# Kernel optimization log

Hardware: AMD Instinct MI355X
Metric: run time of the kernel (lower is better)

## Reference

```python
import jax, jax.numpy as jnp
import numpy as np

EPS = 1e-6
NHEADS = 16


def setup_inputs() -> dict:
    key = jax.random.key(0)
    ks = jax.random.split(key, 6)
    b, n, dim, h = 2, 2048, 2048, NHEADS
    d = dim // h
    x = jax.random.normal(ks[0], (b, n, dim), dtype=jnp.float32)
    qkv_w = jax.random.normal(ks[1], (3 * dim, dim), dtype=jnp.float32) * (dim ** -0.5)
    qkv_b = jax.random.normal(ks[2], (3 * dim,), dtype=jnp.float32) * 0.01
    q_norm_w = jnp.ones((d,), dtype=jnp.float32)
    k_norm_w = jnp.ones((d,), dtype=jnp.float32)
    # Flux-style rotation matrices: (1, 1, n, d/2, 2, 2)
    pos = jnp.arange(n, dtype=jnp.float32)[:, None]
    inv_freq = 1.0 / (10000.0 ** (jnp.arange(0, d, 2, dtype=jnp.float32) / d))  # [d/2]
    ang = pos * inv_freq[None, :]  # [n, d/2]
    cos, sin = jnp.cos(ang), jnp.sin(ang)
    rot = jnp.stack([jnp.stack([cos, -sin], axis=-1),
                     jnp.stack([sin, cos], axis=-1)], axis=-1)  # [n, d/2, 2, 2]
    rot = rot[None, None]  # [1,1,n,d/2,2,2]
    return {"x": x, "qkv_w": qkv_w, "qkv_b": qkv_b,
            "q_norm_w": q_norm_w, "k_norm_w": k_norm_w, "rot": rot}


def _rmsnorm(t, w):
    t32 = t.astype(jnp.float32)
    inv = jax.lax.rsqrt(jnp.mean(t32 * t32, axis=-1, keepdims=True) + EPS)
    return ((t32 * inv) * w).astype(t.dtype)


def _apply_rope(t, rot):
    # t: [b,h,n,d]; rot: [1,1,n,d/2,2,2]
    b, h, n, d = t.shape
    tx = t.astype(jnp.float32).reshape(b, h, n, d // 2, 1, 2)
    out = rot[..., 0] * tx[..., 0] + rot[..., 1] * tx[..., 1]  # [b,h,n,d/2,2]
    return out.reshape(b, h, n, d).astype(t.dtype)


def reference(x, qkv_w, qkv_b, q_norm_w, k_norm_w, rot):
    b, n, dim = x.shape
    d = q_norm_w.shape[0]
    h = dim // d
    qkv = x @ qkv_w.T + qkv_b  # [b, n, 3*dim]
    # layout per Rearrange 'b n (h d j) -> b h n d j'
    qkv = qkv.reshape(b, n, h, d, 3).transpose(0, 2, 1, 3, 4)  # [b,h,n,d,3]
    q, k, v = qkv[..., 0], qkv[..., 1], qkv[..., 2]
    q = _apply_rope(_rmsnorm(q, q_norm_w), rot)
    k = _apply_rope(_rmsnorm(k, k_norm_w), rot)
    scores = jnp.einsum('bhqd,bhkd->bhqk', q, k) * (d ** -0.5)
    attn = jax.nn.softmax(scores, axis=-1)
    out = jnp.einsum('bhqk,bhkd->bhqd', attn, v)
    return out.transpose(0, 2, 1, 3).reshape(b, n, dim)  # b n (h d)
```

## Files before the change

kernel.cpp:

```cpp
#include <hip/hip_runtime.h>
#include <cstdint>
#include <cstddef>


#define LOG2E 1.4426950408889634f
#define ATT_SCALE 0.08838834764831845f
#define QSCALE (ATT_SCALE * LOG2E)

typedef __attribute__((ext_vector_type(8))) __bf16 bf16x8;
typedef __attribute__((ext_vector_type(4))) __bf16 bf16x4;
typedef __attribute__((ext_vector_type(4))) float f32x4;

__device__ __forceinline__ float b2f(unsigned u) {
  u <<= 16;
  return __builtin_bit_cast(float, u);
}
__device__ __forceinline__ unsigned short f2b(float f) {
  unsigned x = __builtin_bit_cast(unsigned, f);
  return (unsigned short)((x + 0x7fffu + ((x >> 16) & 1u)) >> 16);
}
__device__ __forceinline__ void gl16(const void* g, void* l) {
  __builtin_amdgcn_global_load_lds((__attribute__((address_space(1))) void*)(g),
                                   (__attribute__((address_space(3))) void*)(l), 16, 0, 0);
}

__global__ void k_cvt(const float4* __restrict__ in, ushort4* __restrict__ out, int n4) {
  int i = blockIdx.x * blockDim.x + threadIdx.x;
  int st = gridDim.x * blockDim.x;
  for (; i < n4; i += st) {
    float4 v = in[i];
    ushort4 o;
    o.x = f2b(v.x); o.y = f2b(v.y); o.z = f2b(v.z); o.w = f2b(v.w);
    out[i] = o;
  }
}

__global__ __launch_bounds__(512, 2) void k_gemm(const unsigned short* __restrict__ A,
                                                 const unsigned short* __restrict__ W,
                                                 const float* __restrict__ bias,
                                                 unsigned short* __restrict__ C) {
  __shared__ __align__(16) unsigned short lds[65536];
  const int tid = threadIdx.x;
  const int w = tid >> 6, l = tid & 63;
  const int lo = l & 15, hi = l >> 4;
  const int WM = w >> 2, WN = w & 3;
  const int wg = blockIdx.x;
  const int swz = (wg & 7) * 64 + (wg >> 3);
  const int mbase = (swz >> 4) * 128, nbase = (swz & 15) * 384;

  const int srow = w * 16 + (l >> 2);
  const int scol = ((l & 3) * 8) ^ (((srow >> 1) & 3) << 3);

  auto stage = [&](int t, int slot) {
    unsigned short* Sa = lds + slot * 16384;
    unsigned short* Sb = Sa + 4096;
    const int kt = t * 32;
    gl16(A + (size_t)(mbase + srow) * 2048 + kt + scol,
         Sa + (w * 16) * 32);
#pragma unroll
    for (int rd = 0; rd < 3; ++rd)
      gl16(W + (size_t)(nbase + rd * 128 + srow) * 2048 + kt + scol,
           Sb + (rd * 128 + w * 16) * 32);
  };

  f32x4 acc[4][6] = {};
  stage(0, 0); stage(1, 1); stage(2, 2);

  const int ea = (hi * 8) ^ (((lo >> 1) & 3) << 3);
  for (int t = 0; t < 64; ++t) {
    if (t < 62)       asm volatile("s_waitcnt vmcnt(8) lgkmcnt(0)" ::: "memory");
    else if (t == 62) asm volatile("s_waitcnt vmcnt(4) lgkmcnt(0)" ::: "memory");
    else              asm volatile("s_waitcnt vmcnt(0) lgkmcnt(0)" ::: "memory");
    __builtin_amdgcn_sched_barrier(0);
    __builtin_amdgcn_s_barrier();
    __builtin_amdgcn_sched_barrier(0);
    if (t + 3 < 64) stage(t + 3, (t + 3) & 3);

    const unsigned short* Sa = lds + (t & 3) * 16384;
    const unsigned short* Sb = Sa + 4096;
    bf16x8 af[4], bf[6];
#pragma unroll
    for (int i = 0; i < 4; ++i)
      af[i] = *(const bf16x8*)&Sa[(WM * 64 + i * 16 + lo) * 32 + ea];
#pragma unroll
    for (int j = 0; j < 6; ++j)
      bf[j] = *(const bf16x8*)&Sb[(WN * 96 + j * 16 + lo) * 32 + ea];

    __builtin_amdgcn_s_setprio(1);
#pragma unroll
    for (int i = 0; i < 4; ++i)
#pragma unroll
      for (int j = 0; j < 6; ++j)
        acc[i][j] = __builtin_amdgcn_mfma_f32_16x16x32_bf16(af[i], bf[j], acc[i][j], 0, 0, 0);
    __builtin_amdgcn_s_setprio(0);
  }

  const int rowb = mbase + WM * 64;
  const int colb = nbase + WN * 96;
#pragma unroll
  for (int j = 0; j < 6; ++j) {
    float bj = bias[colb + j * 16 + lo];
#pragma unroll
    for (int i = 0; i < 4; ++i)
#pragma unroll
      for (int r = 0; r < 4; ++r) {
        int row = rowb + i * 16 + hi * 4 + r;
        C[(size_t)row * 6144 + colb + j * 16 + lo] = f2b(acc[i][j][r] + bj);
      }
  }
}

__global__ __launch_bounds__(256) void k_normrope(const unsigned short* __restrict__ qkv,
                                                  const float* __restrict__ qw,
                                                  const float* __restrict__ kw,
                                                  const float* __restrict__ rot,
                                                  unsigned short* __restrict__ Q,
                                                  unsigned short* __restrict__ K,
                                                  unsigned short* __restrict__ V) {
  const int l = threadIdx.x & 63;
  const int idx = blockIdx.x * 4 + (threadIdx.x >> 6);
  const int h = idx & 15;
  const int n = (idx >> 4) & 2047;
  const int b = idx >> 15;
  const unsigned* p = (const unsigned*)(qkv + (size_t)(b * 2048 + n) * 6144 + h * 384 + l * 6);
  unsigned u0 = p[0], u1 = p[1], u2 = p[2];
  float q0 = b2f(u0 & 0xffff), k0 = b2f(u0 >> 16);
  float v0 = b2f(u1 & 0xffff), q1 = b2f(u1 >> 16);
  float k1 = b2f(u2 & 0xffff), v1 = b2f(u2 >> 16);
  (void)v0; (void)v1;
  float sq = q0 * q0 + q1 * q1, sk = k0 * k0 + k1 * k1;
#pragma unroll
  for (int m = 1; m < 64; m <<= 1) {
    sq += __shfl_xor(sq, m, 64);
    sk += __shfl_xor(sk, m, 64);
  }
  float qi = rsqrtf(sq * (1.0f / 128.0f) + 1e-6f) * QSCALE;
  float ki = rsqrtf(sk * (1.0f / 128.0f) + 1e-6f);
  float2 qwv = *(const float2*)&qw[2 * l];
  float2 kwv = *(const float2*)&kw[2 * l];
  float4 r = *(const float4*)&rot[n * 256 + l * 4];
  float qn0 = q0 * qi * qwv.x, qn1 = q1 * qi * qwv.y;
  float kn0 = k0 * ki * kwv.x, kn1 = k1 * ki * kwv.y;
  unsigned qo = (unsigned)f2b(r.x * qn0 + r.y * qn1) | ((unsigned)f2b(r.z * qn0 + r.w * qn1) << 16);
  unsigned ko = (unsigned)f2b(r.x * kn0 + r.y * kn1) | ((unsigned)f2b(r.z * kn0 + r.w * kn1) << 16);
  unsigned vo = (u1 & 0xffffu) | (u2 & 0xffff0000u);
  size_t ob = ((size_t)(b * 16 + h) * 2048 + n) * 128 + 2 * l;
  *(unsigned*)(Q + ob) = qo;
  *(unsigned*)(K + ob) = ko;
  *(unsigned*)(V + ob) = vo;
}

__global__ __launch_bounds__(256) void k_transpose(const unsigned short* __restrict__ V,
                                                   unsigned short* __restrict__ Vt) {
  __shared__ unsigned short tile[64 * 66];
  const int t = threadIdx.x;
  const int d0 = blockIdx.x * 64;
  const int n0 = blockIdx.y * 64;
  const int bh = blockIdx.z;
#pragma unroll
  for (int s = t; s < 512; s += 256) {
    int nr = s >> 3, c8 = (s & 7) * 8;
    uint4 vv = *(const uint4*)(V + ((size_t)bh * 2048 + n0 + nr) * 128 + d0 + c8);
    unsigned* tp = (unsigned*)&tile[nr * 66 + c8];
    tp[0] = vv.x; tp[1] = vv.y; tp[2] = vv.z; tp[3] = vv.w;
  }
  __syncthreads();
#pragma unroll
  for (int s = t; s < 512; s += 256) {
    int dr = s >> 3, n8 = (s & 7) * 8;
    unsigned short e[8];
#pragma unroll
    for (int j = 0; j < 8; ++j) e[j] = tile[(n8 + j) * 66 + dr];
    uint4 o;
    o.x = e[0] | ((unsigned)e[1] << 16);
    o.y = e[2] | ((unsigned)e[3] << 16);
    o.z = e[4] | ((unsigned)e[5] << 16);
    o.w = e[6] | ((unsigned)e[7] << 16);
    *(uint4*)(Vt + ((size_t)bh * 128 + d0 + dr) * 2048 + n0 + n8) = o;
  }
}

__global__ __launch_bounds__(256, 2) void k_attn(const unsigned short* __restrict__ Q,
                                                 const unsigned short* __restrict__ K,
                                                 const unsigned short* __restrict__ Vt,
                                                 float* __restrict__ out) {
  __shared__ __align__(16) unsigned short lds[40960];
  unsigned short* Ps = lds + 32768;
  const int tid = threadIdx.x;
  const int w = tid >> 6, l = tid & 63;
  const int lo = l & 15, hi = l >> 4;
  const int swz = (lo & 7) << 3;
  const int id = blockIdx.x;
  const int bh = (id & 7) * 4 + ((id >> 3) & 3);
  const int qt = id >> 5;
  const unsigned short* Qb = Q + (size_t)bh * 2048 * 128;
  const unsigned short* Kb = K + (size_t)bh * 2048 * 128;
  const unsigned short* Vb = Vt + (size_t)bh * 128 * 2048;
  unsigned short* Pswa = Ps + w * 2048;
  unsigned short* Pswb = Pswa + 1024;

  bf16x8 qfa[4], qfb[4];
  const int qrow = qt * 128 + w * 32 + lo;
#pragma unroll
  for (int dk = 0; dk < 4; ++dk) {
    qfa[dk] = *(const bf16x8*)&Qb[(size_t)qrow * 128 + dk * 32 + hi * 8];
    qfb[dk] = *(const bf16x8*)&Qb[(size_t)(qrow + 16) * 128 + dk * 32 + hi * 8];
  }

  f32x4 Oa[8] = {}, Ob[8] = {};
  float m_a = -__builtin_inff(), l_a = 0.0f;
  float m_b = -__builtin_inff(), l_b = 0.0f;

  const int krow0 = w * 4 + hi;
  const int vrow0 = w * 8 + (l >> 3);
  const unsigned short* kp = Kb + (size_t)krow0 * 128 + ((lo * 8) ^ ((krow0 & 7) << 3));
  const unsigned short* vp = Vb + (size_t)vrow0 * 2048 + (((l & 7) * 8) ^ ((vrow0 & 7) << 3));

  auto stage = [&](int t, int b) {
    unsigned short* Ksb = lds + b * 16384;
    unsigned short* Vtsb = Ksb + 8192;
#pragma unroll
    for (int r = 0; r < 4; ++r) {
      gl16(kp + (size_t)t * 8192 + r * 2048,
           Ksb + (r * 16 + w * 4) * 128);
      gl16(vp + (size_t)r * 65536 + t * 64,
           Vtsb + (r * 32 + w * 8) * 64);
    }
  };

  auto softmax = [&](f32x4* S, float& m_run, float& l_run, unsigned short* Psw_, f32x4* Oacc) {
    float m01, m23, mt;
    m01 = fmaxf(fmaxf(S[0][0], S[0][1]), fmaxf(S[0][2], S[0][3]));
    m23 = fmaxf(fmaxf(S[1][0], S[1][1]), fmaxf(S[1][2], S[1][3]));
    mt = fmaxf(m01, m23);
    m01 = fmaxf(fmaxf(S[2][0], S[2][1]), fmaxf(S[2][2], S[2][3]));
    m23 = fmaxf(fmaxf(S[3][0], S[3][1]), fmaxf(S[3][2], S[3][3]));
    mt = fmaxf(mt, fmaxf(m01, m23));
    mt = fmaxf(mt, __shfl_xor(mt, 16, 64));
    mt = fmaxf(mt, __shfl_xor(mt, 32, 64));
    const bool defer = __all(mt <= m_run + 8.0f);
    float m_new = m_run, alpha = 1.0f;
    if (!defer) {
      m_new = fmaxf(m_run, mt);
      alpha = exp2f(m_run - m_new);
    }
    float p[4][4];
    float ls = 0.0f;
#pragma unroll
    for (int kf = 0; kf < 4; ++kf)
#pragma unroll
      for (int r = 0; r < 4; ++r) {
        p[kf][r] = exp2f(S[kf][r] - m_new);
        ls += p[kf][r];
      }
    ls += __shfl_xor(ls, 16, 64);
    ls += __shfl_xor(ls, 32, 64);
#pragma unroll
    for (int kf = 0; kf < 4; ++kf) {
      bf16x4 pk;
      pk[0] = (__bf16)p[kf][0]; pk[1] = (__bf16)p[kf][1];
      pk[2] = (__bf16)p[kf][2]; pk[3] = (__bf16)p[kf][3];
      *(bf16x4*)&Psw_[lo * 64 + ((kf * 16 + hi * 4) ^ swz)] = pk;
    }
    if (!defer) {
#pragma unroll
      for (int df = 0; df < 8; ++df) {
        Oacc[df][0] *= alpha; Oacc[df][1] *= alpha;
        Oacc[df][2] *= alpha; Oacc[df][3] *= alpha;
      }
      l_run = l_run * alpha + ls;
      m_run = m_new;
    } else {
      l_run += ls;
    }
  };

  stage(0, 0);
  int cur = 0;
  for (int t = 0; t < 32; ++t) {
    __syncthreads();
    if (t + 1 < 32) stage(t + 1, cur ^ 1);
    const unsigned short* Ks = lds + cur * 16384;
    const unsigned short* Vts = Ks + 8192;

    f32x4 Sa[4] = {}, Sb[4] = {};
#pragma unroll
    for (int kf = 0; kf < 4; ++kf)
#pragma unroll
      for (int dk = 0; dk < 4; ++dk) {
        const bf16x8 kfrag =
            *(const bf16x8*)&Ks[(kf * 16 + lo) * 128 + ((dk * 32 + hi * 8) ^ swz)];
        Sa[kf] = __builtin_amdgcn_mfma_f32_16x16x32_bf16(kfrag, qfa[dk], Sa[kf], 0, 0, 0);
        Sb[kf] = __builtin_amdgcn_mfma_f32_16x16x32_bf16(kfrag, qfb[dk], Sb[kf], 0, 0, 0);
      }

    softmax(Sa, m_a, l_a, Pswa, Oa);
    softmax(Sb, m_b, l_b, Pswb, Ob);

    const bf16x8 pa0 = *(const bf16x8*)&Pswa[lo * 64 + ((hi * 8) ^ swz)];
    const bf16x8 pa1 = *(const bf16x8*)&Pswa[lo * 64 + ((32 + hi * 8) ^ swz)];
    const bf16x8 pb0 = *(const bf16x8*)&Pswb[lo * 64 + ((hi * 8) ^ swz)];
    const bf16x8 pb1 = *(const bf16x8*)&Pswb[lo * 64 + ((32 + hi * 8) ^ swz)];
#pragma unroll
    for (int df = 0; df < 8; ++df) {
      const bf16x8 v0 = *(const bf16x8*)&Vts[(df * 16 + lo) * 64 + ((hi * 8) ^ swz)];
      const bf16x8 v1 = *(const bf16x8*)&Vts[(df * 16 + lo) * 64 + ((32 + hi * 8) ^ swz)];
      Oa[df] = __builtin_amdgcn_mfma_f32_16x16x32_bf16(v0, pa0, Oa[df], 0, 0, 0);
      Oa[df] = __builtin_amdgcn_mfma_f32_16x16x32_bf16(v1, pa1, Oa[df], 0, 0, 0);
      Ob[df] = __builtin_amdgcn_mfma_f32_16x16x32_bf16(v0, pb0, Ob[df], 0, 0, 0);
      Ob[df] = __builtin_amdgcn_mfma_f32_16x16x32_bf16(v1, pb1, Ob[df], 0, 0, 0);
    }
    cur ^= 1;
  }

  const float inva = 1.0f / l_a;
  const float invb = 1.0f / l_b;
  const int b = bh >> 4, h = bh & 15;
  const int q2 = l >> 2, c = (l & 3) * 32;
  float* Ot = ((float*)lds) + w * 2048;

  __syncthreads();
#pragma unroll
  for (int df = 0; df < 8; ++df)
#pragma unroll
    for (int r = 0; r < 4; ++r)
      Ot[lo * 128 + df * 16 + hi * 4 + r] = Oa[df][r] * inva;
  __syncthreads();
  {
    float* op = out + ((size_t)(b * 2048 + qt * 128 + w * 32 + q2) * 2048 + h * 128 + c);
#pragma unroll
    for (int u = 0; u < 8; ++u)
      *(float4*)&op[u * 4] = *(const float4*)&Ot[q2 * 128 + c + u * 4];
  }
  __syncthreads();
#pragma unroll
  for (int df = 0; df < 8; ++df)
#pragma unroll
    for (int r = 0; r < 4; ++r)
      Ot[lo * 128 + df * 16 + hi * 4 + r] = Ob[df][r] * invb;
  __syncthreads();
  {
    float* op = out + ((size_t)(b * 2048 + qt * 128 + w * 32 + 16 + q2) * 2048 + h * 128 + c);
#pragma unroll
    for (int u = 0; u < 8; ++u)
      *(float4*)&op[u * 4] = *(const float4*)&Ot[q2 * 128 + c + u * 4];
  }
}

extern "C" void kernel_launch(void* const* d_in, const int* in_sizes, int n_in,
                              void* d_out, int out_size, void* d_ws, size_t ws_size,
                              hipStream_t stream) {
  (void)in_sizes; (void)n_in; (void)out_size; (void)ws_size;
  const float* x = (const float*)d_in[0];
  const float* qkv_w = (const float*)d_in[1];
  const float* qkv_b = (const float*)d_in[2];
  const float* q_norm_w = (const float*)d_in[3];
  const float* k_norm_w = (const float*)d_in[4];
  const float* rot = (const float*)d_in[5];
  float* out = (float*)d_out;
  char* ws = (char*)d_ws;
  unsigned short* xb  = (unsigned short*)(ws);
  unsigned short* wb  = (unsigned short*)(ws + 16777216);
  unsigned short* qkv = (unsigned short*)(ws + 41943040);
  unsigned short* Qb  = (unsigned short*)(ws + 92274688);
  unsigned short* Kb  = (unsigned short*)(ws + 109051904);
  unsigned short* Vb  = (unsigned short*)(ws + 125829120);
  unsigned short* Vtb = (unsigned short*)(ws);

  hipLaunchKernelGGL(k_cvt, dim3(1024), dim3(256), 0, stream,
                     (const float4*)x, (ushort4*)xb, 8388608 / 4);
  hipLaunchKernelGGL(k_cvt, dim3(1024), dim3(256), 0, stream,
                     (const float4*)qkv_w, (ushort4*)wb, 12582912 / 4);
  hipLaunchKernelGGL(k_gemm, dim3(512), dim3(512), 0, stream, xb, wb, qkv_b, qkv);
  hipLaunchKernelGGL(k_normrope, dim3(16384), dim3(256), 0, stream,
                     qkv, q_norm_w, k_norm_w, rot, Qb, Kb, Vb);
  hipLaunchKernelGGL(k_transpose, dim3(2, 32, 32), dim3(256), 0, stream, Vb, Vtb);
  hipLaunchKernelGGL(k_attn, dim3(512), dim3(256), 0, stream, Qb, Kb, Vtb, out);
}
```

Baseline: 259.4 us.

## Replace online softmax max tracking with static bound from RMSNorm weights

After RMSNorm and RoPE, every q and k row has a bounded norm. A tiny new kernel computes a fixed score upper bound from the norm weights, and attention subtracts that constant instead of tracking a running row max. This removes the per-tile max reductions, the wave vote, the rescaling of O and l, and the per-tile row-sum shuffles, which are now done once at the end. It also pads the LDS output staging rows to 132 floats to avoid bank conflicts. The trade-off is a risk of exp underflow or precision loss if the true scores sit far below the bound, for example with large norm weights.

Measured after the change: 252.8 us (median of 3 runs). 2.5% less time.

```diff
diff --git a/kernel.cpp b/kernel.cpp
--- a/kernel.cpp
+++ b/kernel.cpp
@@ -33,6 +33,20 @@
     o.x = f2b(v.x); o.y = f2b(v.y); o.z = f2b(v.z); o.w = f2b(v.w);
     out[i] = o;
   }
+}
+
+__global__ __launch_bounds__(64) void k_mbound(const float* __restrict__ qw,
+                                               const float* __restrict__ kw,
+                                               float* __restrict__ M) {
+  const int l = threadIdx.x;
+  float mq = fmaxf(fabsf(qw[l]), fabsf(qw[l + 64]));
+  float mk = fmaxf(fabsf(kw[l]), fabsf(kw[l + 64]));
+#pragma unroll
+  for (int m = 1; m < 64; m <<= 1) {
+    mq = fmaxf(mq, __shfl_xor(mq, m, 64));
+    mk = fmaxf(mk, __shfl_xor(mk, m, 64));
+  }
+  if (l == 0) *M = 128.0f * mq * mk * QSCALE;
 }
 
 __global__ __launch_bounds__(512, 2) void k_gemm(const unsigned short* __restrict__ A,
@@ -183,6 +197,7 @@
 __global__ __launch_bounds__(256, 2) void k_attn(const unsigned short* __restrict__ Q,
                                                  const unsigned short* __restrict__ K,
                                                  const unsigned short* __restrict__ Vt,
+                                                 const float* __restrict__ Mp,
                                                  float* __restrict__ out) {
   __shared__ __align__(16) unsigned short lds[40960];
   unsigned short* Ps = lds + 32768;
@@ -190,6 +205,7 @@
   const int w = tid >> 6, l = tid & 63;
   const int lo = l & 15, hi = l >> 4;
   const int swz = (lo & 7) << 3;
+  const float M = *Mp;
   const int id = blockIdx.x;
   const int bh = (id & 7) * 4 + ((id >> 3) & 3);
   const int qt = id >> 5;
@@ -208,8 +224,7 @@
   }
 
   f32x4 Oa[8] = {}, Ob[8] = {};
-  float m_a = -__builtin_inff(), l_a = 0.0f;
-  float m_b = -__builtin_inff(), l_b = 0.0f;
+  float l_a = 0.0f, l_b = 0.0f;
 
   const int krow0 = w * 4 + hi;
   const int vrow0 = w * 8 + (l >> 3);
@@ -228,50 +243,18 @@
     }
   };
 
-  auto softmax = [&](f32x4* S, float& m_run, float& l_run, unsigned short* Psw_, f32x4* Oacc) {
-    float m01, m23, mt;
-    m01 = fmaxf(fmaxf(S[0][0], S[0][1]), fmaxf(S[0][2], S[0][3]));
-    m23 = fmaxf(fmaxf(S[1][0], S[1][1]), fmaxf(S[1][2], S[1][3]));
-    mt = fmaxf(m01, m23);
-    m01 = fmaxf(fmaxf(S[2][0], S[2][1]), fmaxf(S[2][2], S[2][3]));
-    m23 = fmaxf(fmaxf(S[3][0], S[3][1]), fmaxf(S[3][2], S[3][3]));
-    mt = fmaxf(mt, fmaxf(m01, m23));
-    mt = fmaxf(mt, __shfl_xor(mt, 16, 64));
-    mt = fmaxf(mt, __shfl_xor(mt, 32, 64));
-    const bool defer = __all(mt <= m_run + 8.0f);
-    float m_new = m_run, alpha = 1.0f;
-    if (!defer) {
-      m_new = fmaxf(m_run, mt);
-      alpha = exp2f(m_run - m_new);
-    }
-    float p[4][4];
-    float ls = 0.0f;
-#pragma unroll
-    for (int kf = 0; kf < 4; ++kf)
-#pragma unroll
-      for (int r = 0; r < 4; ++r) {
-        p[kf][r] = exp2f(S[kf][r] - m_new);
-        ls += p[kf][r];
-      }
-    ls += __shfl_xor(ls, 16, 64);
-    ls += __shfl_xor(ls, 32, 64);
+  auto pstore = [&](f32x4* S, float& l_part, unsigned short* Psw_) {
 #pragma unroll
     for (int kf = 0; kf < 4; ++kf) {
+      float p0 = exp2f(S[kf][0] - M);
+      float p1 = exp2f(S[kf][1] - M);
+      float p2 = exp2f(S[kf][2] - M);
+      float p3 = exp2f(S[kf][3] - M);
+      l_part += (p0 + p1) + (p2 + p3);
       bf16x4 pk;
-      pk[0] = (__bf16)p[kf][0]; pk[1] = (__bf16)p[kf][1];
-      pk[2] = (__bf16)p[kf][2]; pk[3] = (__bf16)p[kf][3];
+      pk[0] = (__bf16)p0; pk[1] = (__bf16)p1;
+      pk[2] = (__bf16)p2; pk[3] = (__bf16)p3;
       *(bf16x4*)&Psw_[lo * 64 + ((kf * 16 + hi * 4) ^ swz)] = pk;
-    }
-    if (!defer) {
-#pragma unroll
-      for (int df = 0; df < 8; ++df) {
-        Oacc[df][0] *= alpha; Oacc[df][1] *= alpha;
-        Oacc[df][2] *= alpha; Oacc[df][3] *= alpha;
-      }
-      l_run = l_run * alpha + ls;
-      m_run = m_new;
-    } else {
-      l_run += ls;
     }
   };
 
@@ -294,8 +277,8 @@
         Sb[kf] = __builtin_amdgcn_mfma_f32_16x16x32_bf16(kfrag, qfb[dk], Sb[kf], 0, 0, 0);
       }
 
-    softmax(Sa, m_a, l_a, Pswa, Oa);
-    softmax(Sb, m_b, l_b, Pswb, Ob);
+    pstore(Sa, l_a, Pswa);
+    pstore(Sb, l_b, Pswb);
 
     const bf16x8 pa0 = *(const bf16x8*)&Pswa[lo * 64 + ((hi * 8) ^ swz)];
     const bf16x8 pa1 = *(const bf16x8*)&Pswa[lo * 64 + ((32 + hi * 8) ^ swz)];
@@ -313,37 +296,41 @@
     cur ^= 1;
   }
 
+  l_a += __shfl_xor(l_a, 16, 64);
+  l_a += __shfl_xor(l_a, 32, 64);
+  l_b += __shfl_xor(l_b, 16, 64);
+  l_b += __shfl_xor(l_b, 32, 64);
   const float inva = 1.0f / l_a;
   const float invb = 1.0f / l_b;
   const int b = bh >> 4, h = bh & 15;
   const int q2 = l >> 2, c = (l & 3) * 32;
-  float* Ot = ((float*)lds) + w * 2048;
+  float* Ot = ((float*)lds) + w * 2112;
 
   __syncthreads();
 #pragma unroll
   for (int df = 0; df < 8; ++df)
 #pragma unroll
     for (int r = 0; r < 4; ++r)
-      Ot[lo * 128 + df * 16 + hi * 4 + r] = Oa[df][r] * inva;
+      Ot[lo * 132 + df * 16 + hi * 4 + r] = Oa[df][r] * inva;
   __syncthreads();
   {
     float* op = out + ((size_t)(b * 2048 + qt * 128 + w * 32 + q2) * 2048 + h * 128 + c);
 #pragma unroll
     for (int u = 0; u < 8; ++u)
-      *(float4*)&op[u * 4] = *(const float4*)&Ot[q2 * 128 + c + u * 4];
+      *(float4*)&op[u * 4] = *(const float4*)&Ot[q2 * 132 + c + u * 4];
   }
   __syncthreads();
 #pragma unroll
   for (int df = 0; df < 8; ++df)
 #pragma unroll
     for (int r = 0; r < 4; ++r)
-      Ot[lo * 128 + df * 16 + hi * 4 + r] = Ob[df][r] * invb;
+      Ot[lo * 132 + df * 16 + hi * 4 + r] = Ob[df][r] * invb;
   __syncthreads();
   {
     float* op = out + ((size_t)(b * 2048 + qt * 128 + w * 32 + 16 + q2) * 2048 + h * 128 + c);
 #pragma unroll
     for (int u = 0; u < 8; ++u)
-      *(float4*)&op[u * 4] = *(const float4*)&Ot[q2 * 128 + c + u * 4];
+      *(float4*)&op[u * 4] = *(const float4*)&Ot[q2 * 132 + c + u * 4];
   }
 }
 
@@ -366,14 +353,16 @@
   unsigned short* Kb  = (unsigned short*)(ws + 109051904);
   unsigned short* Vb  = (unsigned short*)(ws + 125829120);
   unsigned short* Vtb = (unsigned short*)(ws);
+  float* Mb = (float*)(ws + 16777216);
 
   hipLaunchKernelGGL(k_cvt, dim3(1024), dim3(256), 0, stream,
                      (const float4*)x, (ushort4*)xb, 8388608 / 4);
   hipLaunchKernelGGL(k_cvt, dim3(1024), dim3(256), 0, stream,
                      (const float4*)qkv_w, (ushort4*)wb, 12582912 / 4);
   hipLaunchKernelGGL(k_gemm, dim3(512), dim3(512), 0, stream, xb, wb, qkv_b, qkv);
+  hipLaunchKernelGGL(k_mbound, dim3(1), dim3(64), 0, stream, q_norm_w, k_norm_w, Mb);
   hipLaunchKernelGGL(k_normrope, dim3(16384), dim3(256), 0, stream,
                      qkv, q_norm_w, k_norm_w, rot, Qb, Kb, Vb);
   hipLaunchKernelGGL(k_transpose, dim3(2, 32, 32), dim3(256), 0, stream, Vb, Vtb);
-  hipLaunchKernelGGL(k_attn, dim3(512), dim3(256), 0, stream, Qb, Kb, Vtb, out);
-}
+  hipLaunchKernelGGL(k_attn, dim3(512), dim3(256), 0, stream, Qb, Kb, Vtb, Mb, out);
+}
```
